# Kernel tuning notes

Hardware: AMD Instinct MI355X
Metric: run time of the kernel (lower is better)

The kernel has to match this reference:

```python
import jax, jax.numpy as jnp
import numpy as np

# static sizes from init_kwargs / input_specs
B = 8            # batch elements
NH = 16384       # high_res_points per sample
NL = 2048        # low_res_points per sample
F_HR = 64
F_LR = 128


def setup_inputs() -> dict:
    key = jax.random.key(0)
    k1, k2, k3, k4 = jax.random.split(key, 4)
    x_hr = jax.random.normal(k1, (B * NH, F_HR), jnp.float32)
    pos_hr = jax.random.normal(k2, (B * NH, 3), jnp.float32)
    x_lr = jax.random.normal(k3, (B * NL, F_LR), jnp.float32)
    pos_lr = jax.random.normal(k4, (B * NL, 3), jnp.float32)
    # PyG-style contiguous batch assignment (sorted)
    batch_hr = jnp.repeat(jnp.arange(B, dtype=jnp.int32), NH)
    batch_lr = jnp.repeat(jnp.arange(B, dtype=jnp.int32), NL)
    return dict(x_hr=x_hr, pos_hr=pos_hr, batch_hr=batch_hr,
                x_lr=x_lr, pos_lr=pos_lr, batch_lr=batch_lr)


def _knn1_gather(p_h, p_l, f_l):
    # p_h: [nh,3], p_l: [nl,3], f_l: [nl,F]
    # squared euclidean distances [nh,nl] via (a-b)^2 expansion
    d2 = (jnp.sum(p_h * p_h, axis=-1, keepdims=True)
          - 2.0 * (p_h @ p_l.T)
          + jnp.sum(p_l * p_l, axis=-1)[None, :])
    idx = jnp.argmin(d2, axis=1)            # [nh] nearest low-res index
    return jnp.take(f_l, idx, axis=0)       # k=1 interpolation == pure gather


def reference(x_hr, pos_hr, batch_hr, x_lr, pos_lr, batch_lr):
    nB = x_hr.shape[0] // NH  # static
    out_x = jnp.concatenate([x_hr, pos_hr], axis=1)          # [B*NH, F_HR+3]
    lr_feat = jnp.concatenate([x_lr, pos_lr], axis=1)        # [B*NL, F_LR+3]

    # batch vectors are contiguous repeats -> reshape to [B, n, ...]
    ph = pos_hr.reshape(nB, NH, 3)
    pl = pos_lr.reshape(nB, NL, 3)
    fl = lr_feat.reshape(nB, NL, F_LR + 3)

    interp = jax.vmap(_knn1_gather)(ph, pl, fl)              # [B, NH, F_LR+3]
    interp = interp.reshape(nB * NH, F_LR + 3)

    out_x = jnp.concatenate([out_x, interp], axis=1)         # [B*NH, F_HR+3+F_LR+3]
    return (out_x, jnp.zeros((out_x.shape[0], 3), out_x.dtype), batch_hr)
```

## Files before the change

### kernel.cpp

```cpp
#include <hip/hip_runtime.h>

#define NB    8
#define NH    16384
#define NL    2048
#define F_HR  64
#define F_LR  128
#define OUT_COLS 198

__global__ __launch_bounds__(512, 4) void fused_kernel(
    const float* __restrict__ pos_hr,
    const float* __restrict__ pos_lr,
    const float* __restrict__ x_hr,
    const float* __restrict__ x_lr,
    float* __restrict__ out)
{
    __shared__ float4 cand[NL];
    __shared__ float  pval[8][256];
    __shared__ float  gminL[256];
    __shared__ int    winw[256];
    __shared__ short  plist[8][256];
    __shared__ float  phsx[256], phsy[256], phsz[256];
    __shared__ int    s_idx[256];

    if (blockIdx.x < 512) {
        const int b  = blockIdx.x >> 6;
        const int p0 = blockIdx.x << 8;
        const int w  = threadIdx.x >> 6;
        const int l  = threadIdx.x & 63;

        const float* pl = pos_lr + (size_t)b * NL * 3;
#pragma unroll
        for (int j = threadIdx.x; j < NL; j += 512) {
            float x = pl[j * 3 + 0];
            float y = pl[j * 3 + 1];
            float z = pl[j * 3 + 2];
            cand[j] = make_float4(x, y, z, 0.5f * ((x * x + y * y) + z * z));
        }

        float phx[4], phy[4], phz[4];
#pragma unroll
        for (int m = 0; m < 4; ++m) {
            const int pt = p0 + (m << 6) + l;
            phx[m] = pos_hr[pt * 3 + 0];
            phy[m] = pos_hr[pt * 3 + 1];
            phz[m] = pos_hr[pt * 3 + 2];
        }
        if (w == 0) {
#pragma unroll
            for (int m = 0; m < 4; ++m) {
                const int ptl = (m << 6) + l;
                phsx[ptl] = phx[m]; phsy[ptl] = phy[m]; phsz[ptl] = phz[m];
            }
        }
        __syncthreads();

        float best[4];
#pragma unroll
        for (int m = 0; m < 4; ++m) best[m] = 3.4e38f;

        const int base = w << 8;
#pragma unroll 4
        for (int j = 0; j < 256; j += 2) {
            const float4 c0 = cand[base + j];
            const float4 c1 = cand[base + j + 1];
#pragma unroll
            for (int m = 0; m < 4; ++m) {
                float d0 = fmaf(-phz[m], c0.z, fmaf(-phy[m], c0.y, fmaf(-phx[m], c0.x, c0.w)));
                float d1 = fmaf(-phz[m], c1.z, fmaf(-phy[m], c1.y, fmaf(-phx[m], c1.x, c1.w)));
                best[m] = fminf(fminf(d0, d1), best[m]);
            }
        }
#pragma unroll
        for (int m = 0; m < 4; ++m)
            pval[w][(m << 6) + l] = best[m];
        __syncthreads();

        if (threadIdx.x < 256) {
            const int t = threadIdx.x;
            float g = pval[0][t]; int ww = 0;
#pragma unroll
            for (int q = 1; q < 8; ++q) {
                const float qv = pval[q][t];
                if (qv < g) { g = qv; ww = q; }
            }
            gminL[t] = g; winw[t] = ww;
        }
        __syncthreads();

        int cnt = 0;
#pragma unroll
        for (int m = 0; m < 4; ++m) {
            const int pt = (m << 6) + l;
            const bool pred = (winw[pt] == w);
            const unsigned long long mask = __ballot(pred);
            const int pos = __popcll(mask & ((1ull << l) - 1ull));
            if (pred) plist[w][cnt + pos] = (short)pt;
            cnt += __popcll(mask);
        }

        for (int i = 0; i < cnt; ++i) {
            const int pt = plist[w][i];
            const float qx = phsx[pt], qy = phsy[pt], qz = phsz[pt];
            const float g  = gminL[pt];
            int loc = 4;
#pragma unroll
            for (int k = 3; k >= 0; --k) {
                const float4 c = cand[base + (l << 2) + k];
                const float d = fmaf(-qz, c.z, fmaf(-qy, c.y, fmaf(-qx, c.x, c.w)));
                if (d == g) loc = k;
            }
            const unsigned long long mk = __ballot(loc < 4);
            if (mk) {
                const int firstlane = __ffsll((unsigned long long)mk) - 1;
                const int locf = __shfl(loc, firstlane);
                if (l == 0)
                    s_idx[pt] = b * NL + base + (firstlane << 2) + locf;
            }
        }
        __syncthreads();

        {
            const int tid = threadIdx.x;
            int rl = tid / 131;
            int c  = tid - rl * 131;
            for (int t = 0; t < 11; ++t) {
                int rs[6], cs[6], ls[6];
                float vs[6];
#pragma unroll
                for (int k = 0; k < 6; ++k) {
                    rs[k] = rl; cs[k] = c;
                    ls[k] = s_idx[rl < 256 ? rl : 255];
                    c += 119;
                    const int carry = (c >= 131) ? 1 : 0;
                    c -= carry ? 131 : 0;
                    rl += 3 + carry;
                }
#pragma unroll
                for (int k = 0; k < 6; ++k) {
                    const int cc = cs[k];
                    const float* a = (cc < F_LR) ? x_lr   + ls[k] * F_LR + cc
                                                 : pos_lr + ls[k] * 3    + (cc - F_LR);
                    vs[k] = *a;
                }
#pragma unroll
                for (int k = 0; k < 6; ++k) {
                    if (t == 10 && k == 5 && tid + 33280 >= 33536) continue;
                    out[(size_t)(p0 + rs[k]) * OUT_COLS + 67 + cs[k]] = vs[k];
                }
            }
        }
    } else {
        const int cb = blockIdx.x - 512;
        const int r0 = cb << 9;

#pragma unroll 4
        for (int e = threadIdx.x; e < 512 * 67; e += 512) {
            const int rl  = e / 67;
            const int c   = e - rl * 67;
            const int row = r0 + rl;
            const float v = (c < F_HR) ? x_hr[(row << 6) + c]
                                       : pos_hr[row * 3 + (c - F_HR)];
            out[row * OUT_COLS + c] = v;
        }

        const int R0 = NB * NH * OUT_COLS;
        const int Z  = NB * NH * 3;
        const int z0 = cb << 11;
#pragma unroll
        for (int e = threadIdx.x; e < 2048; e += 512) {
            const int i = z0 + e;
            out[R0 + i] = (i < Z) ? 0.0f : (float)((i - Z) >> 14);
        }
    }
}

extern "C" void kernel_launch(void* const* d_in, const int* in_sizes, int n_in,
                              void* d_out, int out_size, void* d_ws, size_t ws_size,
                              hipStream_t stream) {
    const float* x_hr   = (const float*)d_in[0];
    const float* pos_hr = (const float*)d_in[1];
    const float* x_lr   = (const float*)d_in[3];
    const float* pos_lr = (const float*)d_in[4];

    fused_kernel<<<dim3(768), dim3(512), 0, stream>>>(
        pos_hr, pos_lr, x_hr, x_lr, (float*)d_out);
}
```

Measured before the change: 54.32 us.

## Halve high-res points per block and use shared atomics for cross-wave argmin

Each block now handles 128 high-res points instead of 256, doubling the number of kNN blocks and raising launch-bounds occupancy to 8 blocks per CU. The cross-wave minimum reduction goes through order-preserving float keys with shared-memory atomicMin, replacing the pval staging pass and a serial 8-way compare. The gather loop is resized for 128 rows, with a tail loop for the leftover elements. Every block still loads all 2048 candidate positions into LDS, so that per-point load cost doubles in exchange for more parallelism.

```diff
diff --git a/kernel.cpp b/kernel.cpp
--- a/kernel.cpp
+++ b/kernel.cpp
@@ -7,39 +7,50 @@
 #define F_LR  128
 #define OUT_COLS 198
 
-__global__ __launch_bounds__(512, 4) void fused_kernel(
+__device__ __forceinline__ unsigned fkey(float v) {
+    unsigned b = __float_as_uint(v);
+    return b ^ ((unsigned)((int)b >> 31) | 0x80000000u);
+}
+__device__ __forceinline__ float fdec(unsigned k) {
+    unsigned b = (k & 0x80000000u) ? (k ^ 0x80000000u) : ~k;
+    return __uint_as_float(b);
+}
+
+__global__ __launch_bounds__(512, 8) void fused_kernel(
     const float* __restrict__ pos_hr,
     const float* __restrict__ pos_lr,
     const float* __restrict__ x_hr,
     const float* __restrict__ x_lr,
     float* __restrict__ out)
 {
-    __shared__ float4 cand[NL];
-    __shared__ float  pval[8][256];
-    __shared__ float  gminL[256];
-    __shared__ int    winw[256];
-    __shared__ short  plist[8][256];
-    __shared__ float  phsx[256], phsy[256], phsz[256];
-    __shared__ int    s_idx[256];
-
-    if (blockIdx.x < 512) {
-        const int b  = blockIdx.x >> 6;
-        const int p0 = blockIdx.x << 8;
+    __shared__ float4   cand[NL];
+    __shared__ unsigned gmin[128];
+    __shared__ int      winw[128];
+    __shared__ short    plist[8][128];
+    __shared__ float    phsx[128], phsy[128], phsz[128];
+    __shared__ int      s_idx[128];
+
+    if (blockIdx.x < 1024) {
+        const int b  = blockIdx.x >> 7;
+        const int p0 = blockIdx.x << 7;
         const int w  = threadIdx.x >> 6;
         const int l  = threadIdx.x & 63;
 
         const float* pl = pos_lr + (size_t)b * NL * 3;
-#pragma unroll
         for (int j = threadIdx.x; j < NL; j += 512) {
             float x = pl[j * 3 + 0];
             float y = pl[j * 3 + 1];
             float z = pl[j * 3 + 2];
             cand[j] = make_float4(x, y, z, 0.5f * ((x * x + y * y) + z * z));
         }
-
-        float phx[4], phy[4], phz[4];
-#pragma unroll
-        for (int m = 0; m < 4; ++m) {
+        if (threadIdx.x < 128) {
+            gmin[threadIdx.x] = 0xFFFFFFFFu;
+            winw[threadIdx.x] = 8;
+        }
+
+        float phx[2], phy[2], phz[2];
+#pragma unroll
+        for (int m = 0; m < 2; ++m) {
             const int pt = p0 + (m << 6) + l;
             phx[m] = pos_hr[pt * 3 + 0];
             phy[m] = pos_hr[pt * 3 + 1];
@@ -47,16 +58,15 @@
         }
         if (w == 0) {
 #pragma unroll
-            for (int m = 0; m < 4; ++m) {
+            for (int m = 0; m < 2; ++m) {
                 const int ptl = (m << 6) + l;
                 phsx[ptl] = phx[m]; phsy[ptl] = phy[m]; phsz[ptl] = phz[m];
             }
         }
         __syncthreads();
 
-        float best[4];
-#pragma unroll
-        for (int m = 0; m < 4; ++m) best[m] = 3.4e38f;
+        float best[2];
+        best[0] = 3.4e38f; best[1] = 3.4e38f;
 
         const int base = w << 8;
 #pragma unroll 4
@@ -64,32 +74,31 @@
             const float4 c0 = cand[base + j];
             const float4 c1 = cand[base + j + 1];
 #pragma unroll
-            for (int m = 0; m < 4; ++m) {
+            for (int m = 0; m < 2; ++m) {
                 float d0 = fmaf(-phz[m], c0.z, fmaf(-phy[m], c0.y, fmaf(-phx[m], c0.x, c0.w)));
                 float d1 = fmaf(-phz[m], c1.z, fmaf(-phy[m], c1.y, fmaf(-phx[m], c1.x, c1.w)));
                 best[m] = fminf(fminf(d0, d1), best[m]);
             }
         }
-#pragma unroll
-        for (int m = 0; m < 4; ++m)
-            pval[w][(m << 6) + l] = best[m];
-        __syncthreads();
-
-        if (threadIdx.x < 256) {
-            const int t = threadIdx.x;
-            float g = pval[0][t]; int ww = 0;
-#pragma unroll
-            for (int q = 1; q < 8; ++q) {
-                const float qv = pval[q][t];
-                if (qv < g) { g = qv; ww = q; }
-            }
-            gminL[t] = g; winw[t] = ww;
+
+        unsigned key[2];
+#pragma unroll
+        for (int m = 0; m < 2; ++m) {
+            key[m] = fkey(best[m]);
+            atomicMin(&gmin[(m << 6) + l], key[m]);
+        }
+        __syncthreads();
+
+#pragma unroll
+        for (int m = 0; m < 2; ++m) {
+            const int pt = (m << 6) + l;
+            if (key[m] == gmin[pt]) atomicMin(&winw[pt], w);
         }
         __syncthreads();
 
         int cnt = 0;
 #pragma unroll
-        for (int m = 0; m < 4; ++m) {
+        for (int m = 0; m < 2; ++m) {
             const int pt = (m << 6) + l;
             const bool pred = (winw[pt] == w);
             const unsigned long long mask = __ballot(pred);
@@ -101,7 +110,7 @@
         for (int i = 0; i < cnt; ++i) {
             const int pt = plist[w][i];
             const float qx = phsx[pt], qy = phsy[pt], qz = phsz[pt];
-            const float g  = gminL[pt];
+            const float g  = fdec(gmin[pt]);
             int loc = 4;
 #pragma unroll
             for (int k = 3; k >= 0; --k) {
@@ -123,13 +132,13 @@
             const int tid = threadIdx.x;
             int rl = tid / 131;
             int c  = tid - rl * 131;
-            for (int t = 0; t < 11; ++t) {
+            for (int t = 0; t < 5; ++t) {
                 int rs[6], cs[6], ls[6];
                 float vs[6];
 #pragma unroll
                 for (int k = 0; k < 6; ++k) {
                     rs[k] = rl; cs[k] = c;
-                    ls[k] = s_idx[rl < 256 ? rl : 255];
+                    ls[k] = s_idx[rl];
                     c += 119;
                     const int carry = (c >= 131) ? 1 : 0;
                     c -= carry ? 131 : 0;
@@ -144,13 +153,26 @@
                 }
 #pragma unroll
                 for (int k = 0; k < 6; ++k) {
-                    if (t == 10 && k == 5 && tid + 33280 >= 33536) continue;
                     out[(size_t)(p0 + rs[k]) * OUT_COLS + 67 + cs[k]] = vs[k];
                 }
             }
+#pragma unroll
+            for (int s = 0; s < 3; ++s) {
+                const int e = tid + (30 + s) * 512;
+                if (e < 128 * 131) {
+                    const int ll = s_idx[rl];
+                    const float v = (c < F_LR) ? x_lr[ll * F_LR + c]
+                                               : pos_lr[ll * 3 + (c - F_LR)];
+                    out[(size_t)(p0 + rl) * OUT_COLS + 67 + c] = v;
+                    c += 119;
+                    const int carry = (c >= 131) ? 1 : 0;
+                    c -= carry ? 131 : 0;
+                    rl += 3 + carry;
+                }
+            }
         }
     } else {
-        const int cb = blockIdx.x - 512;
+        const int cb = blockIdx.x - 1024;
         const int r0 = cb << 9;
 
 #pragma unroll 4
@@ -182,6 +204,6 @@
     const float* x_lr   = (const float*)d_in[3];
     const float* pos_lr = (const float*)d_in[4];
 
-    fused_kernel<<<dim3(768), dim3(512), 0, stream>>>(
+    fused_kernel<<<dim3(1280), dim3(512), 0, stream>>>(
         pos_hr, pos_lr, x_hr, x_lr, (float*)d_out);
 }
```

New measurement: 58.54 us. 7.8% more time.

## Double block size to 16 waves and reduce per-point minima with shared atomics

Applied to the files above, without the earlier changes.

Blocks now have 1024 threads, so 16 waves each scan 128 candidates instead of 8 waves scanning 256. This halves the per-wave distance loop. The cross-wave argmin now uses order-preserving uint keys with shared-memory atomicMin for the value and the winning wave, replacing the serial 8-way scan. The gather and copy phases are retiled for the larger block and the grid shrinks to 640 blocks. The risks are lower occupancy from the 1024-thread launch bounds, atomic contention in LDS, and more synchronisation cost per block.

```diff
diff --git a/kernel.cpp b/kernel.cpp
--- a/kernel.cpp
+++ b/kernel.cpp
@@ -7,34 +7,47 @@
 #define F_LR  128
 #define OUT_COLS 198
 
-__global__ __launch_bounds__(512, 4) void fused_kernel(
+__device__ __forceinline__ unsigned fkey(float v) {
+    unsigned b = __float_as_uint(v);
+    return b ^ ((unsigned)((int)b >> 31) | 0x80000000u);
+}
+__device__ __forceinline__ float fdec(unsigned k) {
+    unsigned b = (k & 0x80000000u) ? (k ^ 0x80000000u) : ~k;
+    return __uint_as_float(b);
+}
+
+__global__ __launch_bounds__(1024, 8) void fused_kernel(
     const float* __restrict__ pos_hr,
     const float* __restrict__ pos_lr,
     const float* __restrict__ x_hr,
     const float* __restrict__ x_lr,
     float* __restrict__ out)
 {
-    __shared__ float4 cand[NL];
-    __shared__ float  pval[8][256];
-    __shared__ float  gminL[256];
-    __shared__ int    winw[256];
-    __shared__ short  plist[8][256];
-    __shared__ float  phsx[256], phsy[256], phsz[256];
-    __shared__ int    s_idx[256];
+    __shared__ float4        cand[NL];
+    __shared__ unsigned      gmin[256];
+    __shared__ int           winw[256];
+    __shared__ unsigned char plist[16][256];
+    __shared__ float         phsx[256], phsy[256], phsz[256];
+    __shared__ int           s_idx[256];
+
+    const int tid = threadIdx.x;
 
     if (blockIdx.x < 512) {
         const int b  = blockIdx.x >> 6;
         const int p0 = blockIdx.x << 8;
-        const int w  = threadIdx.x >> 6;
-        const int l  = threadIdx.x & 63;
+        const int w  = tid >> 6;
+        const int l  = tid & 63;
 
         const float* pl = pos_lr + (size_t)b * NL * 3;
-#pragma unroll
-        for (int j = threadIdx.x; j < NL; j += 512) {
+        for (int j = tid; j < NL; j += 1024) {
             float x = pl[j * 3 + 0];
             float y = pl[j * 3 + 1];
             float z = pl[j * 3 + 2];
             cand[j] = make_float4(x, y, z, 0.5f * ((x * x + y * y) + z * z));
+        }
+        if (tid < 256) {
+            gmin[tid] = 0xFFFFFFFFu;
+            winw[tid] = 16;
         }
 
         float phx[4], phy[4], phz[4];
@@ -58,9 +71,9 @@
 #pragma unroll
         for (int m = 0; m < 4; ++m) best[m] = 3.4e38f;
 
-        const int base = w << 8;
+        const int base = w << 7;
 #pragma unroll 4
-        for (int j = 0; j < 256; j += 2) {
+        for (int j = 0; j < 128; j += 2) {
             const float4 c0 = cand[base + j];
             const float4 c1 = cand[base + j + 1];
 #pragma unroll
@@ -70,20 +83,19 @@
                 best[m] = fminf(fminf(d0, d1), best[m]);
             }
         }
+
+        unsigned key[4];
 #pragma unroll
-        for (int m = 0; m < 4; ++m)
-            pval[w][(m << 6) + l] = best[m];
+        for (int m = 0; m < 4; ++m) {
+            key[m] = fkey(best[m]);
+            atomicMin(&gmin[(m << 6) + l], key[m]);
+        }
         __syncthreads();
 
-        if (threadIdx.x < 256) {
-            const int t = threadIdx.x;
-            float g = pval[0][t]; int ww = 0;
 #pragma unroll
-            for (int q = 1; q < 8; ++q) {
-                const float qv = pval[q][t];
-                if (qv < g) { g = qv; ww = q; }
-            }
-            gminL[t] = g; winw[t] = ww;
+        for (int m = 0; m < 4; ++m) {
+            const int pt = (m << 6) + l;
+            if (key[m] == gmin[pt]) atomicMin(&winw[pt], w);
         }
         __syncthreads();
 
@@ -94,67 +106,66 @@
             const bool pred = (winw[pt] == w);
             const unsigned long long mask = __ballot(pred);
             const int pos = __popcll(mask & ((1ull << l) - 1ull));
-            if (pred) plist[w][cnt + pos] = (short)pt;
+            if (pred) plist[w][cnt + pos] = (unsigned char)pt;
             cnt += __popcll(mask);
         }
 
         for (int i = 0; i < cnt; ++i) {
             const int pt = plist[w][i];
             const float qx = phsx[pt], qy = phsy[pt], qz = phsz[pt];
-            const float g  = gminL[pt];
-            int loc = 4;
+            const float g  = fdec(gmin[pt]);
+            int loc = 2;
 #pragma unroll
-            for (int k = 3; k >= 0; --k) {
-                const float4 c = cand[base + (l << 2) + k];
+            for (int k = 1; k >= 0; --k) {
+                const float4 c = cand[base + (l << 1) + k];
                 const float d = fmaf(-qz, c.z, fmaf(-qy, c.y, fmaf(-qx, c.x, c.w)));
                 if (d == g) loc = k;
             }
-            const unsigned long long mk = __ballot(loc < 4);
+            const unsigned long long mk = __ballot(loc < 2);
             if (mk) {
                 const int firstlane = __ffsll((unsigned long long)mk) - 1;
                 const int locf = __shfl(loc, firstlane);
                 if (l == 0)
-                    s_idx[pt] = b * NL + base + (firstlane << 2) + locf;
+                    s_idx[pt] = b * NL + base + (firstlane << 1) + locf;
             }
         }
         __syncthreads();
 
         {
-            const int tid = threadIdx.x;
             int rl = tid / 131;
             int c  = tid - rl * 131;
-            for (int t = 0; t < 11; ++t) {
-                int rs[6], cs[6], ls[6];
-                float vs[6];
+            for (int t = 0; t < 3; ++t) {
+                int rs[11], cs[11], ls[11];
+                float vs[11];
 #pragma unroll
-                for (int k = 0; k < 6; ++k) {
+                for (int k = 0; k < 11; ++k) {
                     rs[k] = rl; cs[k] = c;
                     ls[k] = s_idx[rl < 256 ? rl : 255];
-                    c += 119;
+                    c += 107;
                     const int carry = (c >= 131) ? 1 : 0;
                     c -= carry ? 131 : 0;
-                    rl += 3 + carry;
+                    rl += 7 + carry;
                 }
 #pragma unroll
-                for (int k = 0; k < 6; ++k) {
+                for (int k = 0; k < 11; ++k) {
                     const int cc = cs[k];
                     const float* a = (cc < F_LR) ? x_lr   + ls[k] * F_LR + cc
                                                  : pos_lr + ls[k] * 3    + (cc - F_LR);
                     vs[k] = *a;
                 }
 #pragma unroll
-                for (int k = 0; k < 6; ++k) {
-                    if (t == 10 && k == 5 && tid + 33280 >= 33536) continue;
+                for (int k = 0; k < 11; ++k) {
+                    if (t == 2 && k == 10 && tid >= 768) continue;
                     out[(size_t)(p0 + rs[k]) * OUT_COLS + 67 + cs[k]] = vs[k];
                 }
             }
         }
     } else {
         const int cb = blockIdx.x - 512;
-        const int r0 = cb << 9;
+        const int r0 = cb << 10;
 
 #pragma unroll 4
-        for (int e = threadIdx.x; e < 512 * 67; e += 512) {
+        for (int e = tid; e < 1024 * 67; e += 1024) {
             const int rl  = e / 67;
             const int c   = e - rl * 67;
             const int row = r0 + rl;
@@ -165,9 +176,9 @@
 
         const int R0 = NB * NH * OUT_COLS;
         const int Z  = NB * NH * 3;
-        const int z0 = cb << 11;
+        const int z0 = cb << 12;
 #pragma unroll
-        for (int e = threadIdx.x; e < 2048; e += 512) {
+        for (int e = tid; e < 4096; e += 1024) {
             const int i = z0 + e;
             out[R0 + i] = (i < Z) ? 0.0f : (float)((i - Z) >> 14);
         }
@@ -182,6 +193,6 @@
     const float* x_lr   = (const float*)d_in[3];
     const float* pos_lr = (const float*)d_in[4];
 
-    fused_kernel<<<dim3(768), dim3(512), 0, stream>>>(
+    fused_kernel<<<dim3(640), dim3(1024), 0, stream>>>(
         pos_hr, pos_lr, x_hr, x_lr, (float*)d_out);
 }
```

After: 71.73 us. 32.0% more time.
